# Kernel tuning notes

Measured on AMD Instinct MI355X. Metric: run time of the kernel, lower is better.

The kernel has to match this reference:

```python
import jax, jax.numpy as jnp
import numpy as np

B, L, D = 4, 4096, 1024  # batch, seq_len, d_model


def setup_inputs() -> dict:
    key = jax.random.key(0)
    k0, k1, k2 = jax.random.split(key, 3)
    x = jax.random.normal(k0, (B, L, D), dtype=jnp.float32)
    # Dense(d_model*3) applied to x: kernel [D, 3D], bias [3D]
    W_proj = jax.random.normal(k1, (D, 3 * D), dtype=jnp.float32) / np.sqrt(D)
    b_proj = jnp.zeros((3 * D,), dtype=jnp.float32)
    # Output Dense(d_model): kernel [D, D], bias [D]
    W_out = jax.random.normal(k2, (D, D), dtype=jnp.float32) / np.sqrt(D)
    b_out = jnp.zeros((D,), dtype=jnp.float32)
    return {"x": x, "W_proj": W_proj, "b_proj": b_proj,
            "W_out": W_out, "b_out": b_out,
            "layer_idx": 0, "num_layers": 12}


def reference(x, W_proj, b_proj, W_out, b_out, layer_idx, num_layers):
    # x: [B, L, D] -> x_proj: [B, L, 3D]
    x_proj = jnp.einsum('bld,de->ble', x, W_proj) + b_proj
    gate_input, forget_input, output_gate = jnp.split(x_proj, 3, axis=-1)
    # NOTE: in the source, forget_gate / input_gate / k / v / the lax.scan
    # recurrence are defined but never used to produce the output (dead code).
    # The live path is exactly:
    out = gate_input * jax.nn.sigmoid(output_gate)          # [B, L, D]
    out = jnp.einsum('bld,de->ble', out, W_out) + b_out     # [B, L, D]
    # Dropout is deterministic (training=False) -> identity.
    return out
```

## Files before the change

### kernel.cpp

```cpp
#include <hip/hip_runtime.h>
#include <hip/hip_bf16.h>


#define MTOT 16384
#define DM   1024
#define MEG  (1024 * 1024)

typedef __bf16 bf16x8 __attribute__((ext_vector_type(8)));
typedef float  f32x4  __attribute__((ext_vector_type(4)));

#define AS1 __attribute__((address_space(1)))
#define AS3 __attribute__((address_space(3)))

static __device__ __forceinline__ void async_load16(const void* g, void* l) {
    __builtin_amdgcn_global_load_lds((const AS1 void*)g, (AS3 void*)l, 16, 0, 0);
}

static __device__ __forceinline__ unsigned short f2bf(float f) {
    __hip_bfloat16 h = __float2bfloat16(f);
    return *(unsigned short*)&h;
}

__global__ __launch_bounds__(256)
void conv_x(const float* __restrict__ x, unsigned short* __restrict__ dst) {
    const size_t i = ((size_t)blockIdx.x * 256 + threadIdx.x) * 8;
    const f32x4 a = *(const f32x4*)(x + i);
    const f32x4 b = *(const f32x4*)(x + i + 4);
    __align__(16) unsigned short o[8];
    o[0] = f2bf(a[0]); o[1] = f2bf(a[1]); o[2] = f2bf(a[2]); o[3] = f2bf(a[3]);
    o[4] = f2bf(b[0]); o[5] = f2bf(b[1]); o[6] = f2bf(b[2]); o[7] = f2bf(b[3]);
    *(uint4*)(dst + i) = *(const uint4*)o;
}

__global__ void transpose_w(const float* __restrict__ Wproj, const float* __restrict__ Wout,
                            unsigned short* __restrict__ dst0) {
    __shared__ unsigned short t[32][33];
    const int z = blockIdx.z;
    const float* src;
    unsigned short* dst;
    int ld, coff;
    if (z == 0)      { src = Wproj; ld = 3072; coff = 0;    dst = dst0; }
    else if (z == 1) { src = Wproj; ld = 3072; coff = 2048; dst = dst0 + MEG; }
    else             { src = Wout;  ld = 1024; coff = 0;    dst = dst0 + 2 * MEG; }
    const int k0 = blockIdx.x * 32;
    const int n0 = blockIdx.y * 32;
    const int tx = threadIdx.x, ty = threadIdx.y;
    for (int i = ty; i < 32; i += 8)
        t[i][tx] = f2bf(src[(size_t)(k0 + i) * ld + coff + n0 + tx]);
    __syncthreads();
    for (int i = ty; i < 32; i += 8)
        dst[(size_t)(n0 + i) * DM + k0 + tx] = t[tx][i];
}

__global__ __launch_bounds__(512)
void gemm1_fused(const unsigned short* __restrict__ X,
                 const unsigned short* __restrict__ WgT,
                 const unsigned short* __restrict__ WoT,
                 const float* __restrict__ bproj,
                 unsigned short* __restrict__ Hlo,
                 unsigned short* __restrict__ Hhi) {
    __shared__ __align__(16) unsigned short sA[2][256 * 64];
    __shared__ __align__(16) unsigned short sB[2][256 * 64];

    const int tid  = threadIdx.x;
    const int wave = tid >> 6;
    const int lane = tid & 63;
    const int wm = wave & 1;
    const int wn = wave >> 1;

    const int bid = blockIdx.x;
    const int swz = (bid & 7) * 64 + (bid >> 3);
    const int m0 = (swz >> 3) * 256;
    const int n0 = (swz & 7) * 128;

    unsigned short* __restrict__ H =
        (m0 < 8192) ? Hlo : (Hhi - (size_t)8192 * DM);

    const int rA = lane & 15;
    const int qq = lane >> 4;
    const int r7 = rA & 7;
    const int swq   = ((qq ^ (r7 & 3)) << 4);
    const int k0off = ((rA >> 2) & 1) << 6;
    const int k1off = k0off ^ 64;
    const int ldsA_base = (wm * 64 + rA) * 128 + swq;
    const int ldsB_base = (wn * 16 + rA) * 128 + swq;

    const int trow = tid >> 3;
    const int tsw  = (((tid & 7) ^ (trow & 7)) << 4);
    const char* srcA  = (const char*)X   + (size_t)(m0 + trow) * 2048 + tsw;
    const char* srcBg = (const char*)WgT + (size_t)(n0 + trow) * 2048 + tsw;
    const char* srcBo = (const char*)WoT + (size_t)(n0 + trow) * 2048 + tsw;
    char* dA = (char*)&sA[0][0] + tid * 16;
    char* dB = (char*)&sB[0][0] + tid * 16;

#define STA1(b, kt, r)  async_load16(srcA  + (kt) * 128 + (r) * 131072, dA + (b) * 32768 + (r) * 8192)
#define STBG1(b, kt, r) async_load16(srcBg + (kt) * 128 + (r) * 131072, dB + (b) * 32768 + (r) * 8192)
#define STBO1(b, kt, r) async_load16(srcBo + (kt) * 128 + (r) * 131072, dB + (b) * 32768 + (2 + (r)) * 8192)
#define LDA1(dst, bb, h, il, kof) dst = *(const bf16x8*)((const char*)sA + (bb) * 32768 + ldsA_base + (h) * 16384 + (il) * 2048 + (kof))
#define LDB1(dst, bb, mat, j, kof) dst = *(const bf16x8*)((const char*)sB + (bb) * 32768 + ldsB_base + (mat) * 16384 + (j) * 8192 + (kof))

    f32x4 aG[2][4][2], aO[2][4][2];
    bf16x8 fa[4][2], fbg[2][2], fbo[2][2];

    STA1(0, 0, 0); STA1(0, 0, 1); STA1(0, 0, 2); STA1(0, 0, 3);
    STBG1(0, 0, 0); STBG1(0, 0, 1); STBO1(0, 0, 0); STBO1(0, 0, 1);
    STA1(1, 1, 0); STA1(1, 1, 1); STBG1(1, 1, 0); STBO1(1, 1, 0);

#pragma unroll
    for (int h = 0; h < 2; ++h)
#pragma unroll
        for (int il = 0; il < 4; ++il)
#pragma unroll
            for (int jl = 0; jl < 2; ++jl) {
                aG[h][il][jl] = (f32x4){0.f, 0.f, 0.f, 0.f};
                aO[h][il][jl] = (f32x4){0.f, 0.f, 0.f, 0.f};
            }

    asm volatile("s_waitcnt vmcnt(4)" ::: "memory");
    __builtin_amdgcn_s_barrier();

#define MM1(H_) do { \
    _Pragma("unroll") \
    for (int kk = 0; kk < 2; ++kk) \
        _Pragma("unroll") \
        for (int il = 0; il < 4; ++il) \
            _Pragma("unroll") \
            for (int jl = 0; jl < 2; ++jl) { \
                aG[H_][il][jl] = __builtin_amdgcn_mfma_f32_16x16x32_bf16(fa[il][kk], fbg[jl][kk], aG[H_][il][jl], 0, 0, 0); \
                aO[H_][il][jl] = __builtin_amdgcn_mfma_f32_16x16x32_bf16(fa[il][kk], fbo[jl][kk], aO[H_][il][jl], 0, 0, 0); \
            } } while (0)

#define TILE1(kt, b, nb) do { \
     \
    _Pragma("unroll") \
    for (int il = 0; il < 4; ++il) { LDA1(fa[il][0], b, 0, il, k0off); LDA1(fa[il][1], b, 0, il, k1off); } \
    _Pragma("unroll") \
    for (int jl = 0; jl < 2; ++jl) { \
        LDB1(fbg[jl][0], b, 0, jl, k0off); LDB1(fbg[jl][1], b, 0, jl, k1off); \
        LDB1(fbo[jl][0], b, 1, jl, k0off); LDB1(fbo[jl][1], b, 1, jl, k1off); } \
    if ((kt) < 15) { STA1(nb, (kt) + 1, 2); STA1(nb, (kt) + 1, 3); STBG1(nb, (kt) + 1, 1); STBO1(nb, (kt) + 1, 1); } \
    asm volatile("s_waitcnt lgkmcnt(0)" ::: "memory"); \
    __builtin_amdgcn_sched_barrier(0); \
    __builtin_amdgcn_s_setprio(1); MM1(0); __builtin_amdgcn_s_setprio(0); \
    __builtin_amdgcn_s_barrier(); \
     \
    _Pragma("unroll") \
    for (int il = 0; il < 4; ++il) { LDA1(fa[il][0], b, 1, il, k0off); LDA1(fa[il][1], b, 1, il, k1off); } \
    if ((kt) < 14) { STA1(b, (kt) + 2, 0); STA1(b, (kt) + 2, 1); STBG1(b, (kt) + 2, 0); STBO1(b, (kt) + 2, 0); } \
    asm volatile("s_waitcnt lgkmcnt(0)" ::: "memory"); \
    __builtin_amdgcn_sched_barrier(0); \
    __builtin_amdgcn_s_setprio(1); MM1(1); __builtin_amdgcn_s_setprio(0); \
    if ((kt) < 14) { asm volatile("s_waitcnt vmcnt(4)" ::: "memory"); } \
    else           { asm volatile("s_waitcnt vmcnt(0)" ::: "memory"); } \
    __builtin_amdgcn_s_barrier(); \
} while (0)

#pragma unroll 1
    for (int kt2 = 0; kt2 < 16; kt2 += 2) {
        TILE1(kt2, 0, 1);
        TILE1(kt2 + 1, 1, 0);
    }
#undef TILE1
#undef MM1
#undef STA1
#undef STBG1
#undef STBO1
#undef LDA1
#undef LDB1

    const int colL = lane & 15;
    const int rowQ = (lane >> 4) * 4;
#pragma unroll
    for (int jl = 0; jl < 2; ++jl) {
        const int n = n0 + wn * 16 + jl * 64 + colL;
        const float bgv = bproj[n];
        const float bov = bproj[2048 + n];
#pragma unroll
        for (int h = 0; h < 2; ++h)
#pragma unroll
            for (int il = 0; il < 4; ++il) {
                const int mbase = m0 + wm * 64 + h * 128 + il * 16 + rowQ;
#pragma unroll
                for (int r = 0; r < 4; ++r) {
                    const float g = aG[h][il][jl][r] + bgv;
                    const float o = aO[h][il][jl][r] + bov;
                    const float hv = g * (1.0f / (1.0f + __expf(-o)));
                    H[(size_t)(mbase + r) * DM + n] = f2bf(hv);
                }
            }
    }
}

__global__ __launch_bounds__(512)
void gemm2(const unsigned short* __restrict__ Hlo,
           const unsigned short* __restrict__ Hhi,
           const unsigned short* __restrict__ Bt,
           const float* __restrict__ bout,
           float* __restrict__ Out,
           int row_base) {
    __shared__ __align__(16) unsigned short sA[2][256 * 64];
    __shared__ __align__(16) unsigned short sB[2][128 * 64];

    const int tid  = threadIdx.x;
    const int wave = tid >> 6;
    const int lane = tid & 63;
    const int wm = wave & 3;
    const int wn = wave >> 2;

    const int bid = blockIdx.x;
    const int q8  = (int)gridDim.x >> 3;
    const int swz = (bid & 7) * q8 + (bid >> 3);
    const int m0 = row_base + (swz >> 3) * 256;
    const int n0 = (swz & 7) * 128;

    const unsigned short* __restrict__ A =
        (m0 < 8192) ? (Hlo + (size_t)m0 * DM) : (Hhi + (size_t)(m0 - 8192) * DM);

    const int rA = lane & 15;
    const int qq = lane >> 4;
    const int r7 = rA & 7;
    const int swq   = ((qq ^ (r7 & 3)) << 4);
    const int k0off = ((rA >> 2) & 1) << 6;
    const int k1off = k0off ^ 64;
    const int ldsA_base = (wm * 64 + rA) * 128 + swq;
    const int ldsB_base = (wn * 64 + rA) * 128 + swq;

    const int trow = tid >> 3;
    const int tsw  = (((tid & 7) ^ (trow & 7)) << 4);
    const char* srcA = (const char*)A  + (size_t)trow * 2048 + tsw;
    const char* srcB = (const char*)Bt + (size_t)(n0 + trow) * 2048 + tsw;
    char* dA = (char*)&sA[0][0] + tid * 16;
    char* dB = (char*)&sB[0][0] + tid * 16;

#define STA2(b, kt, r) async_load16(srcA + (kt) * 128 + (r) * 131072, dA + (b) * 32768 + (r) * 8192)
#define STB2(b, kt, r) async_load16(srcB + (kt) * 128 + (r) * 131072, dB + (b) * 16384 + (r) * 8192)
#define LDA2(dst, bb, il, kof) dst = *(const bf16x8*)((const char*)sA + (bb) * 32768 + ldsA_base + (il) * 2048 + (kof))
#define LDB2(dst, bb, jl, kof) dst = *(const bf16x8*)((const char*)sB + (bb) * 16384 + ldsB_base + (jl) * 2048 + (kof))

    f32x4 acc[4][4];
    bf16x8 fa[4][2], fb[4][2];

    STA2(0, 0, 0); STA2(0, 0, 1); STA2(0, 0, 2); STA2(0, 0, 3);
    STB2(0, 0, 0); STB2(0, 0, 1);
    STA2(1, 1, 0); STA2(1, 1, 1); STB2(1, 1, 0);

#pragma unroll
    for (int il = 0; il < 4; ++il)
#pragma unroll
        for (int j = 0; j < 4; ++j) acc[il][j] = (f32x4){0.f, 0.f, 0.f, 0.f};

    asm volatile("s_waitcnt vmcnt(3)" ::: "memory");
    __builtin_amdgcn_s_barrier();

#define MM2(JB) do { \
    _Pragma("unroll") \
    for (int kk = 0; kk < 2; ++kk) \
        _Pragma("unroll") \
        for (int il = 0; il < 4; ++il) { \
            acc[il][JB]     = __builtin_amdgcn_mfma_f32_16x16x32_bf16(fa[il][kk], fb[JB][kk],     acc[il][JB],     0, 0, 0); \
            acc[il][JB + 1] = __builtin_amdgcn_mfma_f32_16x16x32_bf16(fa[il][kk], fb[JB + 1][kk], acc[il][JB + 1], 0, 0, 0); \
        } } while (0)

#define TILE2(kt, b, nb) do { \
     \
    _Pragma("unroll") \
    for (int il = 0; il < 4; ++il) { LDA2(fa[il][0], b, il, k0off); LDA2(fa[il][1], b, il, k1off); } \
    _Pragma("unroll") \
    for (int jl = 0; jl < 4; ++jl) { LDB2(fb[jl][0], b, jl, k0off); LDB2(fb[jl][1], b, jl, k1off); } \
    if ((kt) < 15) { STA2(nb, (kt) + 1, 2); STA2(nb, (kt) + 1, 3); STB2(nb, (kt) + 1, 1); } \
    asm volatile("s_waitcnt lgkmcnt(0)" ::: "memory"); \
    __builtin_amdgcn_sched_barrier(0); \
    __builtin_amdgcn_s_setprio(1); MM2(0); __builtin_amdgcn_s_setprio(0); \
    __builtin_amdgcn_s_barrier(); \
     \
    if ((kt) < 14) { STA2(b, (kt) + 2, 0); STA2(b, (kt) + 2, 1); STB2(b, (kt) + 2, 0); } \
    __builtin_amdgcn_s_setprio(1); MM2(2); __builtin_amdgcn_s_setprio(0); \
    if ((kt) < 14) { asm volatile("s_waitcnt vmcnt(3)" ::: "memory"); } \
    else           { asm volatile("s_waitcnt vmcnt(0)" ::: "memory"); } \
    __builtin_amdgcn_s_barrier(); \
} while (0)

#pragma unroll 1
    for (int kt2 = 0; kt2 < 16; kt2 += 2) {
        TILE2(kt2, 0, 1);
        TILE2(kt2 + 1, 1, 0);
    }
#undef TILE2
#undef MM2
#undef STA2
#undef STB2
#undef LDA2
#undef LDB2

    const int colL = lane & 15;
    const int rowQ = (lane >> 4) * 4;
#pragma unroll
    for (int jl = 0; jl < 4; ++jl) {
        const int n = n0 + wn * 64 + jl * 16 + colL;
        const float bv = bout[n];
#pragma unroll
        for (int il = 0; il < 4; ++il) {
            const int mbase = m0 + wm * 64 + il * 16 + rowQ;
#pragma unroll
            for (int r = 0; r < 4; ++r)
                Out[(size_t)(mbase + r) * DM + n] = acc[il][jl][r] + bv;
        }
    }
}

extern "C" void kernel_launch(void* const* d_in, const int* in_sizes, int n_in,
                              void* d_out, int out_size, void* d_ws, size_t ws_size,
                              hipStream_t stream) {
    const float* x     = (const float*)d_in[0];
    const float* Wproj = (const float*)d_in[1];
    const float* bproj = (const float*)d_in[2];
    const float* Wout  = (const float*)d_in[3];
    const float* bout  = (const float*)d_in[4];
    float* out = (float*)d_out;

    unsigned short* Xb  = (unsigned short*)d_out;
    unsigned short* WgT   = (unsigned short*)d_ws;
    unsigned short* WoT   = WgT + MEG;
    unsigned short* WoutT = WgT + 2 * MEG;
    unsigned short* Hws   = WgT + 3 * MEG;

    const bool big_ws = ws_size >= (size_t)19 * MEG * 2;

    unsigned short* Hlo = big_ws ? Hws : ((unsigned short*)d_out + 16 * MEG);
    unsigned short* Hhi = big_ws ? (Hws + (size_t)8192 * DM) : Hws;

    conv_x<<<(MTOT * DM) / (256 * 8), 256, 0, stream>>>(x, Xb);

    transpose_w<<<dim3(32, 32, 3), dim3(32, 8, 1), 0, stream>>>(Wproj, Wout, WgT);

    gemm1_fused<<<512, 512, 0, stream>>>(Xb, WgT, WoT, bproj, Hlo, Hhi);

    if (big_ws) {
        gemm2<<<512, 512, 0, stream>>>(Hlo, Hhi, WoutT, bout, out, 0);
    } else {
        gemm2<<<256, 512, 0, stream>>>(Hlo, Hhi, WoutT, bout, out, 0);
        gemm2<<<256, 512, 0, stream>>>(Hlo, Hhi, WoutT, bout, out, 8192);
    }
}
```

Before: 248.4 us.

## Split gemm1 MFMA phases per gate and shrink gemm2 tiles to 128x128

```diff
diff --git a/kernel.cpp b/kernel.cpp
--- a/kernel.cpp
+++ b/kernel.cpp
@@ -119,37 +119,56 @@
     asm volatile("s_waitcnt vmcnt(4)" ::: "memory");
     __builtin_amdgcn_s_barrier();
 
-#define MM1(H_) do { \
+#define MMG1(H_) do { \
     _Pragma("unroll") \
     for (int kk = 0; kk < 2; ++kk) \
         _Pragma("unroll") \
         for (int il = 0; il < 4; ++il) \
             _Pragma("unroll") \
-            for (int jl = 0; jl < 2; ++jl) { \
+            for (int jl = 0; jl < 2; ++jl) \
                 aG[H_][il][jl] = __builtin_amdgcn_mfma_f32_16x16x32_bf16(fa[il][kk], fbg[jl][kk], aG[H_][il][jl], 0, 0, 0); \
+    } while (0)
+#define MMO1(H_) do { \
+    _Pragma("unroll") \
+    for (int kk = 0; kk < 2; ++kk) \
+        _Pragma("unroll") \
+        for (int il = 0; il < 4; ++il) \
+            _Pragma("unroll") \
+            for (int jl = 0; jl < 2; ++jl) \
                 aO[H_][il][jl] = __builtin_amdgcn_mfma_f32_16x16x32_bf16(fa[il][kk], fbo[jl][kk], aO[H_][il][jl], 0, 0, 0); \
-            } } while (0)
+    } while (0)
+
+#define LGKM_SGB() \
+    asm volatile("s_waitcnt lgkmcnt(0)" ::: "memory"); \
+    __builtin_amdgcn_sched_barrier(0)
 
 #define TILE1(kt, b, nb) do { \
      \
     _Pragma("unroll") \
     for (int il = 0; il < 4; ++il) { LDA1(fa[il][0], b, 0, il, k0off); LDA1(fa[il][1], b, 0, il, k1off); } \
     _Pragma("unroll") \
-    for (int jl = 0; jl < 2; ++jl) { \
-        LDB1(fbg[jl][0], b, 0, jl, k0off); LDB1(fbg[jl][1], b, 0, jl, k1off); \
-        LDB1(fbo[jl][0], b, 1, jl, k0off); LDB1(fbo[jl][1], b, 1, jl, k1off); } \
-    if ((kt) < 15) { STA1(nb, (kt) + 1, 2); STA1(nb, (kt) + 1, 3); STBG1(nb, (kt) + 1, 1); STBO1(nb, (kt) + 1, 1); } \
-    asm volatile("s_waitcnt lgkmcnt(0)" ::: "memory"); \
-    __builtin_amdgcn_sched_barrier(0); \
-    __builtin_amdgcn_s_setprio(1); MM1(0); __builtin_amdgcn_s_setprio(0); \
+    for (int jl = 0; jl < 2; ++jl) { LDB1(fbg[jl][0], b, 0, jl, k0off); LDB1(fbg[jl][1], b, 0, jl, k1off); } \
+    if ((kt) < 15) { STA1(nb, (kt) + 1, 2); STA1(nb, (kt) + 1, 3); } \
+    LGKM_SGB(); \
+    __builtin_amdgcn_s_setprio(1); MMG1(0); __builtin_amdgcn_s_setprio(0); \
+    __builtin_amdgcn_s_barrier(); \
+     \
+    _Pragma("unroll") \
+    for (int jl = 0; jl < 2; ++jl) { LDB1(fbo[jl][0], b, 1, jl, k0off); LDB1(fbo[jl][1], b, 1, jl, k1off); } \
+    if ((kt) < 15) { STBG1(nb, (kt) + 1, 1); STBO1(nb, (kt) + 1, 1); } \
+    LGKM_SGB(); \
+    __builtin_amdgcn_s_setprio(1); MMO1(0); __builtin_amdgcn_s_setprio(0); \
     __builtin_amdgcn_s_barrier(); \
      \
     _Pragma("unroll") \
     for (int il = 0; il < 4; ++il) { LDA1(fa[il][0], b, 1, il, k0off); LDA1(fa[il][1], b, 1, il, k1off); } \
-    if ((kt) < 14) { STA1(b, (kt) + 2, 0); STA1(b, (kt) + 2, 1); STBG1(b, (kt) + 2, 0); STBO1(b, (kt) + 2, 0); } \
-    asm volatile("s_waitcnt lgkmcnt(0)" ::: "memory"); \
-    __builtin_amdgcn_sched_barrier(0); \
-    __builtin_amdgcn_s_setprio(1); MM1(1); __builtin_amdgcn_s_setprio(0); \
+    if ((kt) < 14) { STA1(b, (kt) + 2, 0); STA1(b, (kt) + 2, 1); } \
+    LGKM_SGB(); \
+    __builtin_amdgcn_s_setprio(1); MMG1(1); __builtin_amdgcn_s_setprio(0); \
+    __builtin_amdgcn_s_barrier(); \
+     \
+    if ((kt) < 14) { STBG1(b, (kt) + 2, 0); STBO1(b, (kt) + 2, 0); } \
+    __builtin_amdgcn_s_setprio(1); MMO1(1); __builtin_amdgcn_s_setprio(0); \
     if ((kt) < 14) { asm volatile("s_waitcnt vmcnt(4)" ::: "memory"); } \
     else           { asm volatile("s_waitcnt vmcnt(0)" ::: "memory"); } \
     __builtin_amdgcn_s_barrier(); \
@@ -161,7 +180,8 @@
         TILE1(kt2 + 1, 1, 0);
     }
 #undef TILE1
-#undef MM1
+#undef MMG1
+#undef MMO1
 #undef STA1
 #undef STBG1
 #undef STBO1
@@ -191,26 +211,26 @@
     }
 }
 
-__global__ __launch_bounds__(512)
+__global__ __launch_bounds__(256)
 void gemm2(const unsigned short* __restrict__ Hlo,
            const unsigned short* __restrict__ Hhi,
            const unsigned short* __restrict__ Bt,
            const float* __restrict__ bout,
            float* __restrict__ Out,
            int row_base) {
-    __shared__ __align__(16) unsigned short sA[2][256 * 64];
+    __shared__ __align__(16) unsigned short sA[2][128 * 64];
     __shared__ __align__(16) unsigned short sB[2][128 * 64];
 
     const int tid  = threadIdx.x;
     const int wave = tid >> 6;
     const int lane = tid & 63;
-    const int wm = wave & 3;
-    const int wn = wave >> 2;
+    const int wm = wave & 1;
+    const int wn = wave >> 1;
 
     const int bid = blockIdx.x;
     const int q8  = (int)gridDim.x >> 3;
     const int swz = (bid & 7) * q8 + (bid >> 3);
-    const int m0 = row_base + (swz >> 3) * 256;
+    const int m0 = row_base + (swz >> 3) * 128;
     const int n0 = (swz & 7) * 128;
 
     const unsigned short* __restrict__ A =
@@ -232,24 +252,24 @@
     char* dA = (char*)&sA[0][0] + tid * 16;
     char* dB = (char*)&sB[0][0] + tid * 16;
 
-#define STA2(b, kt, r) async_load16(srcA + (kt) * 128 + (r) * 131072, dA + (b) * 32768 + (r) * 8192)
-#define STB2(b, kt, r) async_load16(srcB + (kt) * 128 + (r) * 131072, dB + (b) * 16384 + (r) * 8192)
-#define LDA2(dst, bb, il, kof) dst = *(const bf16x8*)((const char*)sA + (bb) * 32768 + ldsA_base + (il) * 2048 + (kof))
+#define STA2(b, kt, r) async_load16(srcA + (kt) * 128 + (r) * 65536, dA + (b) * 16384 + (r) * 4096)
+#define STB2(b, kt, r) async_load16(srcB + (kt) * 128 + (r) * 65536, dB + (b) * 16384 + (r) * 4096)
+#define LDA2(dst, bb, il, kof) dst = *(const bf16x8*)((const char*)sA + (bb) * 16384 + ldsA_base + (il) * 2048 + (kof))
 #define LDB2(dst, bb, jl, kof) dst = *(const bf16x8*)((const char*)sB + (bb) * 16384 + ldsB_base + (jl) * 2048 + (kof))
 
     f32x4 acc[4][4];
     bf16x8 fa[4][2], fb[4][2];
 
     STA2(0, 0, 0); STA2(0, 0, 1); STA2(0, 0, 2); STA2(0, 0, 3);
-    STB2(0, 0, 0); STB2(0, 0, 1);
-    STA2(1, 1, 0); STA2(1, 1, 1); STB2(1, 1, 0);
+    STB2(0, 0, 0); STB2(0, 0, 1); STB2(0, 0, 2); STB2(0, 0, 3);
+    STA2(1, 1, 0); STA2(1, 1, 1); STB2(1, 1, 0); STB2(1, 1, 2);
 
 #pragma unroll
     for (int il = 0; il < 4; ++il)
 #pragma unroll
         for (int j = 0; j < 4; ++j) acc[il][j] = (f32x4){0.f, 0.f, 0.f, 0.f};
 
-    asm volatile("s_waitcnt vmcnt(3)" ::: "memory");
+    asm volatile("s_waitcnt vmcnt(4)" ::: "memory");
     __builtin_amdgcn_s_barrier();
 
 #define MM2(JB) do { \
@@ -266,16 +286,20 @@
     _Pragma("unroll") \
     for (int il = 0; il < 4; ++il) { LDA2(fa[il][0], b, il, k0off); LDA2(fa[il][1], b, il, k1off); } \
     _Pragma("unroll") \
-    for (int jl = 0; jl < 4; ++jl) { LDB2(fb[jl][0], b, jl, k0off); LDB2(fb[jl][1], b, jl, k1off); } \
-    if ((kt) < 15) { STA2(nb, (kt) + 1, 2); STA2(nb, (kt) + 1, 3); STB2(nb, (kt) + 1, 1); } \
+    for (int jl = 0; jl < 2; ++jl) { LDB2(fb[jl][0], b, jl, k0off); LDB2(fb[jl][1], b, jl, k1off); } \
+    if ((kt) < 15) { STA2(nb, (kt) + 1, 2); STA2(nb, (kt) + 1, 3); STB2(nb, (kt) + 1, 1); STB2(nb, (kt) + 1, 3); } \
     asm volatile("s_waitcnt lgkmcnt(0)" ::: "memory"); \
     __builtin_amdgcn_sched_barrier(0); \
     __builtin_amdgcn_s_setprio(1); MM2(0); __builtin_amdgcn_s_setprio(0); \
     __builtin_amdgcn_s_barrier(); \
      \
-    if ((kt) < 14) { STA2(b, (kt) + 2, 0); STA2(b, (kt) + 2, 1); STB2(b, (kt) + 2, 0); } \
+    _Pragma("unroll") \
+    for (int jl = 2; jl < 4; ++jl) { LDB2(fb[jl][0], b, jl, k0off); LDB2(fb[jl][1], b, jl, k1off); } \
+    if ((kt) < 14) { STA2(b, (kt) + 2, 0); STA2(b, (kt) + 2, 1); STB2(b, (kt) + 2, 0); STB2(b, (kt) + 2, 2); } \
+    asm volatile("s_waitcnt lgkmcnt(0)" ::: "memory"); \
+    __builtin_amdgcn_sched_barrier(0); \
     __builtin_amdgcn_s_setprio(1); MM2(2); __builtin_amdgcn_s_setprio(0); \
-    if ((kt) < 14) { asm volatile("s_waitcnt vmcnt(3)" ::: "memory"); } \
+    if ((kt) < 14) { asm volatile("s_waitcnt vmcnt(4)" ::: "memory"); } \
     else           { asm volatile("s_waitcnt vmcnt(0)" ::: "memory"); } \
     __builtin_amdgcn_s_barrier(); \
 } while (0)
@@ -336,9 +360,9 @@
     gemm1_fused<<<512, 512, 0, stream>>>(Xb, WgT, WoT, bproj, Hlo, Hhi);
 
     if (big_ws) {
-        gemm2<<<512, 512, 0, stream>>>(Hlo, Hhi, WoutT, bout, out, 0);
+        gemm2<<<1024, 256, 0, stream>>>(Hlo, Hhi, WoutT, bout, out, 0);
     } else {
-        gemm2<<<256, 512, 0, stream>>>(Hlo, Hhi, WoutT, bout, out, 0);
-        gemm2<<<256, 512, 0, stream>>>(Hlo, Hhi, WoutT, bout, out, 8192);
-    }
-}
+        gemm2<<<512, 256, 0, stream>>>(Hlo, Hhi, WoutT, bout, out, 0);
+        gemm2<<<512, 256, 0, stream>>>(Hlo, Hhi, WoutT, bout, out, 8192);
+    }
+}
```

New measurement: 238.6 us. 1.04x faster.

## Enlarge gemm2 block tile to 256x256 and halve the grid

Applied to the files above, without the earlier changes.

```diff
diff --git a/kernel.cpp b/kernel.cpp
--- a/kernel.cpp
+++ b/kernel.cpp
@@ -131,7 +131,6 @@
             } } while (0)
 
 #define TILE1(kt, b, nb) do { \
-     \
     _Pragma("unroll") \
     for (int il = 0; il < 4; ++il) { LDA1(fa[il][0], b, 0, il, k0off); LDA1(fa[il][1], b, 0, il, k1off); } \
     _Pragma("unroll") \
@@ -143,7 +142,6 @@
     __builtin_amdgcn_sched_barrier(0); \
     __builtin_amdgcn_s_setprio(1); MM1(0); __builtin_amdgcn_s_setprio(0); \
     __builtin_amdgcn_s_barrier(); \
-     \
     _Pragma("unroll") \
     for (int il = 0; il < 4; ++il) { LDA1(fa[il][0], b, 1, il, k0off); LDA1(fa[il][1], b, 1, il, k1off); } \
     if ((kt) < 14) { STA1(b, (kt) + 2, 0); STA1(b, (kt) + 2, 1); STBG1(b, (kt) + 2, 0); STBO1(b, (kt) + 2, 0); } \
@@ -199,19 +197,19 @@
            float* __restrict__ Out,
            int row_base) {
     __shared__ __align__(16) unsigned short sA[2][256 * 64];
-    __shared__ __align__(16) unsigned short sB[2][128 * 64];
+    __shared__ __align__(16) unsigned short sB[2][256 * 64];
 
     const int tid  = threadIdx.x;
     const int wave = tid >> 6;
     const int lane = tid & 63;
-    const int wm = wave & 3;
-    const int wn = wave >> 2;
+    const int wm = wave & 1;
+    const int wn = wave >> 1;
 
     const int bid = blockIdx.x;
     const int q8  = (int)gridDim.x >> 3;
     const int swz = (bid & 7) * q8 + (bid >> 3);
-    const int m0 = row_base + (swz >> 3) * 256;
-    const int n0 = (swz & 7) * 128;
+    const int m0 = row_base + (swz >> 2) * 256;
+    const int n0 = (swz & 3) * 256;
 
     const unsigned short* __restrict__ A =
         (m0 < 8192) ? (Hlo + (size_t)m0 * DM) : (Hhi + (size_t)(m0 - 8192) * DM);
@@ -223,7 +221,7 @@
     const int k0off = ((rA >> 2) & 1) << 6;
     const int k1off = k0off ^ 64;
     const int ldsA_base = (wm * 64 + rA) * 128 + swq;
-    const int ldsB_base = (wn * 64 + rA) * 128 + swq;
+    const int ldsB_base = (wn * 16 + rA) * 128 + swq;
 
     const int trow = tid >> 3;
     const int tsw  = (((tid & 7) ^ (trow & 7)) << 4);
@@ -233,49 +231,57 @@
     char* dB = (char*)&sB[0][0] + tid * 16;
 
 #define STA2(b, kt, r) async_load16(srcA + (kt) * 128 + (r) * 131072, dA + (b) * 32768 + (r) * 8192)
-#define STB2(b, kt, r) async_load16(srcB + (kt) * 128 + (r) * 131072, dB + (b) * 16384 + (r) * 8192)
-#define LDA2(dst, bb, il, kof) dst = *(const bf16x8*)((const char*)sA + (bb) * 32768 + ldsA_base + (il) * 2048 + (kof))
-#define LDB2(dst, bb, jl, kof) dst = *(const bf16x8*)((const char*)sB + (bb) * 16384 + ldsB_base + (jl) * 2048 + (kof))
-
-    f32x4 acc[4][4];
+#define STB2(b, kt, r) async_load16(srcB + (kt) * 128 + (r) * 131072, dB + (b) * 32768 + (r) * 8192)
+#define LDA2(dst, bb, h, il, kof) dst = *(const bf16x8*)((const char*)sA + (bb) * 32768 + ldsA_base + (h) * 16384 + (il) * 2048 + (kof))
+#define LDB2(dst, bb, jl, kof)    dst = *(const bf16x8*)((const char*)sB + (bb) * 32768 + ldsB_base + (jl) * 8192 + (kof))
+
+    f32x4 acc[2][4][4];
     bf16x8 fa[4][2], fb[4][2];
 
     STA2(0, 0, 0); STA2(0, 0, 1); STA2(0, 0, 2); STA2(0, 0, 3);
-    STB2(0, 0, 0); STB2(0, 0, 1);
-    STA2(1, 1, 0); STA2(1, 1, 1); STB2(1, 1, 0);
-
-#pragma unroll
-    for (int il = 0; il < 4; ++il)
-#pragma unroll
-        for (int j = 0; j < 4; ++j) acc[il][j] = (f32x4){0.f, 0.f, 0.f, 0.f};
-
-    asm volatile("s_waitcnt vmcnt(3)" ::: "memory");
+    STB2(0, 0, 0); STB2(0, 0, 1); STB2(0, 0, 2); STB2(0, 0, 3);
+    STA2(1, 1, 0); STA2(1, 1, 1); STB2(1, 1, 0); STB2(1, 1, 1);
+
+#pragma unroll
+    for (int h = 0; h < 2; ++h)
+#pragma unroll
+        for (int il = 0; il < 4; ++il)
+#pragma unroll
+            for (int jl = 0; jl < 4; ++jl)
+                acc[h][il][jl] = (f32x4){0.f, 0.f, 0.f, 0.f};
+
+    asm volatile("s_waitcnt vmcnt(4)" ::: "memory");
     __builtin_amdgcn_s_barrier();
 
-#define MM2(JB) do { \
+#define MM2(H_) do { \
     _Pragma("unroll") \
     for (int kk = 0; kk < 2; ++kk) \
         _Pragma("unroll") \
-        for (int il = 0; il < 4; ++il) { \
-            acc[il][JB]     = __builtin_amdgcn_mfma_f32_16x16x32_bf16(fa[il][kk], fb[JB][kk],     acc[il][JB],     0, 0, 0); \
-            acc[il][JB + 1] = __builtin_amdgcn_mfma_f32_16x16x32_bf16(fa[il][kk], fb[JB + 1][kk], acc[il][JB + 1], 0, 0, 0); \
-        } } while (0)
+        for (int il = 0; il < 4; ++il) \
+            _Pragma("unroll") \
+            for (int jl = 0; jl < 4; ++jl) \
+                acc[H_][il][jl] = __builtin_amdgcn_mfma_f32_16x16x32_bf16(fa[il][kk], fb[jl][kk], acc[H_][il][jl], 0, 0, 0); \
+    } while (0)
 
 #define TILE2(kt, b, nb) do { \
      \
     _Pragma("unroll") \
-    for (int il = 0; il < 4; ++il) { LDA2(fa[il][0], b, il, k0off); LDA2(fa[il][1], b, il, k1off); } \
+    for (int il = 0; il < 4; ++il) { LDA2(fa[il][0], b, 0, il, k0off); LDA2(fa[il][1], b, 0, il, k1off); } \
     _Pragma("unroll") \
     for (int jl = 0; jl < 4; ++jl) { LDB2(fb[jl][0], b, jl, k0off); LDB2(fb[jl][1], b, jl, k1off); } \
-    if ((kt) < 15) { STA2(nb, (kt) + 1, 2); STA2(nb, (kt) + 1, 3); STB2(nb, (kt) + 1, 1); } \
+    if ((kt) < 15) { STA2(nb, (kt) + 1, 2); STA2(nb, (kt) + 1, 3); STB2(nb, (kt) + 1, 2); STB2(nb, (kt) + 1, 3); } \
     asm volatile("s_waitcnt lgkmcnt(0)" ::: "memory"); \
     __builtin_amdgcn_sched_barrier(0); \
     __builtin_amdgcn_s_setprio(1); MM2(0); __builtin_amdgcn_s_setprio(0); \
     __builtin_amdgcn_s_barrier(); \
      \
-    if ((kt) < 14) { STA2(b, (kt) + 2, 0); STA2(b, (kt) + 2, 1); STB2(b, (kt) + 2, 0); } \
-    __builtin_amdgcn_s_setprio(1); MM2(2); __builtin_amdgcn_s_setprio(0); \
-    if ((kt) < 14) { asm volatile("s_waitcnt vmcnt(3)" ::: "memory"); } \
+    _Pragma("unroll") \
+    for (int il = 0; il < 4; ++il) { LDA2(fa[il][0], b, 1, il, k0off); LDA2(fa[il][1], b, 1, il, k1off); } \
+    if ((kt) < 14) { STA2(b, (kt) + 2, 0); STA2(b, (kt) + 2, 1); STB2(b, (kt) + 2, 0); STB2(b, (kt) + 2, 1); } \
+    asm volatile("s_waitcnt lgkmcnt(0)" ::: "memory"); \
+    __builtin_amdgcn_sched_barrier(0); \
+    __builtin_amdgcn_s_setprio(1); MM2(1); __builtin_amdgcn_s_setprio(0); \
+    if ((kt) < 14) { asm volatile("s_waitcnt vmcnt(4)" ::: "memory"); } \
     else           { asm volatile("s_waitcnt vmcnt(0)" ::: "memory"); } \
     __builtin_amdgcn_s_barrier(); \
 } while (0)
@@ -296,15 +302,17 @@
     const int rowQ = (lane >> 4) * 4;
 #pragma unroll
     for (int jl = 0; jl < 4; ++jl) {
-        const int n = n0 + wn * 64 + jl * 16 + colL;
+        const int n = n0 + wn * 16 + jl * 64 + colL;
         const float bv = bout[n];
 #pragma unroll
-        for (int il = 0; il < 4; ++il) {
-            const int mbase = m0 + wm * 64 + il * 16 + rowQ;
-#pragma unroll
-            for (int r = 0; r < 4; ++r)
-                Out[(size_t)(mbase + r) * DM + n] = acc[il][jl][r] + bv;
-        }
+        for (int h = 0; h < 2; ++h)
+#pragma unroll
+            for (int il = 0; il < 4; ++il) {
+                const int mbase = m0 + wm * 64 + h * 128 + il * 16 + rowQ;
+#pragma unroll
+                for (int r = 0; r < 4; ++r)
+                    Out[(size_t)(mbase + r) * DM + n] = acc[h][il][jl][r] + bv;
+            }
     }
 }
 
@@ -336,9 +344,9 @@
     gemm1_fused<<<512, 512, 0, stream>>>(Xb, WgT, WoT, bproj, Hlo, Hhi);
 
     if (big_ws) {
-        gemm2<<<512, 512, 0, stream>>>(Hlo, Hhi, WoutT, bout, out, 0);
+        gemm2<<<256, 512, 0, stream>>>(Hlo, Hhi, WoutT, bout, out, 0);
     } else {
-        gemm2<<<256, 512, 0, stream>>>(Hlo, Hhi, WoutT, bout, out, 0);
-        gemm2<<<256, 512, 0, stream>>>(Hlo, Hhi, WoutT, bout, out, 8192);
-    }
-}
+        gemm2<<<128, 512, 0, stream>>>(Hlo, Hhi, WoutT, bout, out, 0);
+        gemm2<<<128, 512, 0, stream>>>(Hlo, Hhi, WoutT, bout, out, 8192);
+    }
+}
```

Result: faster. 238.9 us (-3.8%).
